# Performance work log

Measured on AMD Instinct MI355X. Metric: run time of the kernel, lower is better.

Reference implementation:

```python
import jax, jax.numpy as jnp
import numpy as np
import math

D_MODEL = 1024
N_HEADS = 16
HEAD_DIM = D_MODEL // N_HEADS


def setup_inputs() -> dict:
    key = jax.random.key(0)
    k1, k2, k3 = jax.random.split(key, 3)
    B, T = 2, 2048
    x = jax.random.normal(k1, (B, T, D_MODEL), dtype=jnp.float32)
    W_qkv = jax.random.normal(k2, (D_MODEL, 3 * D_MODEL), dtype=jnp.float32) * (1.0 / math.sqrt(D_MODEL))
    W_out = jax.random.normal(k3, (D_MODEL, D_MODEL), dtype=jnp.float32) * (1.0 / math.sqrt(D_MODEL))
    return {"x": x, "W_qkv": W_qkv, "W_out": W_out}


def reference(x, W_qkv, W_out):
    B, T, C = x.shape
    qkv = x @ W_qkv  # [B, T, 3C]
    q, k, v = jnp.split(qkv, 3, axis=-1)

    def heads(t):  # [B,T,C] -> [B,H,T,Dh]
        return t.reshape(B, T, N_HEADS, HEAD_DIM).transpose(0, 2, 1, 3)

    q, k, v = heads(q), heads(k), heads(v)
    scale = 1.0 / math.sqrt(HEAD_DIM)
    scores = jnp.einsum('bhtd,bhsd->bhts', q, k) * scale  # [B,H,T,T]
    causal = jnp.tril(jnp.ones((T, T), dtype=bool))
    scores = jnp.where(causal[None, None, :, :], scores, -jnp.inf)
    attn = jax.nn.softmax(scores, axis=-1)
    out = jnp.einsum('bhts,bhsd->bhtd', attn, v)  # [B,H,T,Dh]
    out = out.transpose(0, 2, 1, 3).reshape(B, T, C)
    return out @ W_out
```

## Files before the change

kernel.cpp:

```cpp
#include <hip/hip_runtime.h>
#include <hip/hip_bf16.h>

typedef __bf16 bf16;
typedef bf16 bf16x4 __attribute__((ext_vector_type(4)));
typedef bf16 bf16x8 __attribute__((ext_vector_type(8)));
typedef float f32x4 __attribute__((ext_vector_type(4)));
typedef float f32x16 __attribute__((ext_vector_type(16)));
typedef unsigned int u32x4 __attribute__((ext_vector_type(4)));

#define GLOAD16(g, l) __builtin_amdgcn_global_load_lds( \
    (const __attribute__((address_space(1))) void*)(g),  \
    (__attribute__((address_space(3))) void*)(l), 16, 0, 0)

#define EXP2F(x) __builtin_amdgcn_exp2f(x)
#define MFMA16(a, b, c) __builtin_amdgcn_mfma_f32_16x16x32_bf16(a, b, c, 0, 0, 0)
#define MFMA32(a, b, c) __builtin_amdgcn_mfma_f32_32x32x16_bf16(a, b, c, 0, 0, 0)

__global__ __launch_bounds__(256) void prep(const float* __restrict__ x,
                                            const float* __restrict__ Wqkv,
                                            const float* __restrict__ Wout,
                                            bf16* __restrict__ xb,
                                            bf16* __restrict__ wqkvT,
                                            bf16* __restrict__ woutT) {
  int id = blockIdx.x, tid = threadIdx.x;
  if (id < 2048) {
    int i = id * 256 + tid;
    const float4* p = (const float4*)x + (size_t)i * 2;
    float4 a = p[0], b = p[1];
    bf16x8 o;
    o[0] = (bf16)a.x; o[1] = (bf16)a.y; o[2] = (bf16)a.z; o[3] = (bf16)a.w;
    o[4] = (bf16)b.x; o[5] = (bf16)b.y; o[6] = (bf16)b.z; o[7] = (bf16)b.w;
    ((bf16x8*)xb)[i] = o;
  } else {
    __shared__ float tile[32][33];
    const float* src; bf16* dst; int N, j;
    if (id < 5120) { src = Wqkv; dst = wqkvT; N = 3072; j = id - 2048; }
    else           { src = Wout; dst = woutT; N = 1024; j = id - 5120; }
    int ntile = N / 32;
    int n0 = (j % ntile) * 32, k0 = (j / ntile) * 32;
    int tx = tid & 31, ty = tid >> 5;
#pragma unroll
    for (int i = 0; i < 4; i++)
      tile[ty + 8 * i][tx] = src[(size_t)(k0 + ty + 8 * i) * N + n0 + tx];
    __syncthreads();
#pragma unroll
    for (int i = 0; i < 4; i++)
      dst[(size_t)(n0 + ty + 8 * i) * 1024 + k0 + tx] = (bf16)tile[tx][ty + 8 * i];
  }
}

__device__ __forceinline__ void gemm_mainloop64(const bf16* __restrict__ A,
                                                const bf16* __restrict__ Bt,
                                                int K, int m0, int n0,
                                                f32x4 acc[4][4],
                                                bf16* As, bf16* Bs) {
  int tid = threadIdx.x;
  int lane = tid & 63;
  int wave = tid >> 6;
  int wr = wave >> 1, wc = wave & 1;
  int c16 = lane & 15, g = lane >> 4;
  f32x4 z = {0.f, 0.f, 0.f, 0.f};
#pragma unroll
  for (int m = 0; m < 4; m++)
#pragma unroll
    for (int n = 0; n < 4; n++) acc[m][n] = z;
  for (int k0 = 0; k0 < K; k0 += 64) {
#pragma unroll
    for (int i = 0; i < 4; i++) {
      int cc = tid + i * 256;
      int r = cc >> 3, ch = cc & 7;
      int sc = ch ^ (r & 7);
      GLOAD16(A + (size_t)(m0 + r) * K + k0 + sc * 8, As + cc * 8);
    }
#pragma unroll
    for (int i = 0; i < 4; i++) {
      int cc = tid + i * 256;
      int r = cc >> 3, ch = cc & 7;
      int sc = ch ^ (r & 7);
      GLOAD16(Bt + (size_t)(n0 + r) * K + k0 + sc * 8, Bs + cc * 8);
    }
    __syncthreads();
#pragma unroll
    for (int h = 0; h < 2; h++) {
      bf16x8 af[4], bfr[4];
#pragma unroll
      for (int m = 0; m < 4; m++) {
        int ar = wr * 64 + m * 16 + c16;
        af[m] = *(const bf16x8*)((const char*)As + ar * 128 + (((h * 4 + g) ^ (ar & 7)) << 4));
      }
#pragma unroll
      for (int n = 0; n < 4; n++) {
        int br = wc * 64 + n * 16 + c16;
        bfr[n] = *(const bf16x8*)((const char*)Bs + br * 128 + (((h * 4 + g) ^ (br & 7)) << 4));
      }
      __builtin_amdgcn_s_setprio(1);
#pragma unroll
      for (int m = 0; m < 4; m++)
#pragma unroll
        for (int n = 0; n < 4; n++)
          acc[m][n] = MFMA16(af[m], bfr[n], acc[m][n]);
      __builtin_amdgcn_s_setprio(0);
    }
    __syncthreads();
  }
}

__global__ __launch_bounds__(256) void gemm_qkv(const bf16* __restrict__ A,
                                                const bf16* __restrict__ Bt,
                                                bf16* __restrict__ q,
                                                bf16* __restrict__ kk,
                                                bf16* __restrict__ vt) {
  __shared__ bf16 As[128 * 64];
  __shared__ bf16 Bs[128 * 64];
  int id = blockIdx.x;
  int xc = id & 7, k = id >> 3;
  int bn = xc * 3 + (k % 3), bm = k / 3;
  int m0 = bm * 128, n0 = bn * 128;
  f32x4 acc[4][4];
  gemm_mainloop64(A, Bt, 1024, m0, n0, acc, As, Bs);
  int lane = threadIdx.x & 63;
  int wave = threadIdx.x >> 6;
  int wr = wave >> 1, wc = wave & 1;
  int c16 = lane & 15, g = lane >> 4;
  int which = n0 >> 10;
  const float QSCALE = 0.125f * 1.4426950408889634f;
  if (which == 2) {
#pragma unroll
    for (int m = 0; m < 4; m++)
#pragma unroll
      for (int n = 0; n < 4; n++) {
        int gm0 = m0 + wr * 64 + m * 16 + g * 4;
        int gn = n0 + wc * 64 + n * 16 + c16;
        int rem = gn & 1023, h = rem >> 6, d = rem & 63;
        int b = gm0 >> 11, t0 = gm0 & 2047;
        size_t bh = (size_t)(b * 16 + h);
        bf16x4 pv;
        pv[0] = (bf16)acc[m][n][0]; pv[1] = (bf16)acc[m][n][1];
        pv[2] = (bf16)acc[m][n][2]; pv[3] = (bf16)acc[m][n][3];
        *(bf16x4*)(vt + (bh * 64 + d) * 2048 + t0) = pv;
      }
  } else {
#pragma unroll
    for (int m = 0; m < 4; m++)
#pragma unroll
      for (int n = 0; n < 4; n++)
#pragma unroll
        for (int j = 0; j < 4; j++) {
          int gm = m0 + wr * 64 + m * 16 + g * 4 + j;
          int gn = n0 + wc * 64 + n * 16 + c16;
          int rem = gn & 1023, h = rem >> 6, d = rem & 63;
          int b = gm >> 11, t = gm & 2047;
          float v = acc[m][n][j];
          size_t bh = (size_t)(b * 16 + h);
          if (which == 0) q[(bh * 2048 + t) * 64 + d]  = (bf16)(v * QSCALE);
          else            kk[(bh * 2048 + t) * 64 + d] = (bf16)v;
        }
  }
}

__global__ __launch_bounds__(256) void gemm_out(const bf16* __restrict__ A,
                                                const bf16* __restrict__ Bt,
                                                float* __restrict__ C) {
  __shared__ bf16 As[64 * 64];
  __shared__ bf16 Bs[128 * 64];
  int tid = threadIdx.x;
  int lane = tid & 63;
  int wave = tid >> 6;
  int wr = wave >> 1, wc = wave & 1;
  int c16 = lane & 15, g = lane >> 4;
  int id = blockIdx.x;
  int bn = id & 7, bm = id >> 3;
  int m0 = bm * 64, n0 = bn * 128;
  const int K = 1024;
  f32x4 acc[2][4];
  {
    f32x4 z = {0.f, 0.f, 0.f, 0.f};
#pragma unroll
    for (int m = 0; m < 2; m++)
#pragma unroll
      for (int n = 0; n < 4; n++) acc[m][n] = z;
  }
  for (int k0 = 0; k0 < K; k0 += 64) {
#pragma unroll
    for (int i = 0; i < 2; i++) {
      int cc = tid + i * 256;
      int r = cc >> 3, ch = cc & 7;
      int sc = ch ^ (r & 7);
      GLOAD16(A + (size_t)(m0 + r) * K + k0 + sc * 8, As + cc * 8);
    }
#pragma unroll
    for (int i = 0; i < 4; i++) {
      int cc = tid + i * 256;
      int r = cc >> 3, ch = cc & 7;
      int sc = ch ^ (r & 7);
      GLOAD16(Bt + (size_t)(n0 + r) * K + k0 + sc * 8, Bs + cc * 8);
    }
    __syncthreads();
#pragma unroll
    for (int h = 0; h < 2; h++) {
      bf16x8 af[2], bfr[4];
#pragma unroll
      for (int m = 0; m < 2; m++) {
        int ar = wr * 32 + m * 16 + c16;
        af[m] = *(const bf16x8*)((const char*)As + ar * 128 + (((h * 4 + g) ^ (ar & 7)) << 4));
      }
#pragma unroll
      for (int n = 0; n < 4; n++) {
        int br = wc * 64 + n * 16 + c16;
        bfr[n] = *(const bf16x8*)((const char*)Bs + br * 128 + (((h * 4 + g) ^ (br & 7)) << 4));
      }
      __builtin_amdgcn_s_setprio(1);
#pragma unroll
      for (int m = 0; m < 2; m++)
#pragma unroll
        for (int n = 0; n < 4; n++)
          acc[m][n] = MFMA16(af[m], bfr[n], acc[m][n]);
      __builtin_amdgcn_s_setprio(0);
    }
    __syncthreads();
  }
#pragma unroll
  for (int m = 0; m < 2; m++)
#pragma unroll
    for (int n = 0; n < 4; n++)
#pragma unroll
      for (int j = 0; j < 4; j++) {
        int gm = m0 + wr * 32 + m * 16 + g * 4 + j;
        int gn = n0 + wc * 64 + n * 16 + c16;
        C[(size_t)gm * 1024 + gn] = acc[m][n][j];
      }
}

__global__ __launch_bounds__(512, 4) void attn(const bf16* __restrict__ q,
                                               const bf16* __restrict__ kk,
                                               const bf16* __restrict__ vt,
                                               bf16* __restrict__ out) {
  __shared__ __align__(16) char smem[65536];
  bf16* Ks = (bf16*)smem;
  bf16* Vs = (bf16*)(smem + 32768);
  int tid = threadIdx.x, lane = tid & 63, w = tid >> 6;
  int qw = w & 3, par = w >> 2;
  int ql = lane & 31, hi = lane >> 5;

  int id = blockIdx.x;
  int c = id & 7;
  int k = id >> 3;
  int s = k >> 5;
  int j5 = k & 31;
  int bxi = j5 & 15, b2 = j5 >> 4;
  int bx = s ? (15 - bxi) : bxi;
  int bh = 4 * c + 2 * b2 + s;
  int q0 = bx * 128;

  const bf16* qb = q  + (size_t)bh * 2048 * 64;
  const bf16* kb = kk + (size_t)bh * 2048 * 64;
  const bf16* vb = vt + (size_t)bh * 64 * 2048;
  int nt = 2 * bx + 2;
  int ns = nt >> 1;

  int qlo = q0 + qw * 32;
  int qg = qlo + ql;

  bf16x8 qf[4];
#pragma unroll
  for (int j = 0; j < 4; j++)
    qf[j] = *(const bf16x8*)(qb + (size_t)qg * 64 + j * 16 + hi * 8);

  {
    int cc = tid;
    int r = cc >> 3;
    int sw = ((cc & 7) ^ (r & 7)) * 8;
    GLOAD16(kb + (size_t)r * 64 + sw, Ks + cc * 8);
    GLOAD16(vb + (size_t)r * 2048 + sw, Vs + cc * 8);
    GLOAD16(kb + (size_t)(64 + r) * 64 + sw, Ks + 4096 + cc * 8);
    GLOAD16(vb + (size_t)r * 2048 + 64 + sw, Vs + 4096 + cc * 8);
  }
  __syncthreads();

  f32x16 o[2];
#pragma unroll
  for (int i = 0; i < 16; i++) { o[0][i] = 0.f; o[1][i] = 0.f; }
  float lsum = 0.f;

  for (int st = 0; st < ns; ++st) {
    if (st + 1 < ns) {
      int sn = st * 128 + 128;
      int nb = (2 * st + 2) & 3;
      int cc = tid;
      int r = cc >> 3;
      int sw = ((cc & 7) ^ (r & 7)) * 8;
      GLOAD16(kb + (size_t)(sn + r) * 64 + sw, Ks + nb * 4096 + cc * 8);
      GLOAD16(vb + (size_t)r * 2048 + sn + sw, Vs + nb * 4096 + cc * 8);
      GLOAD16(kb + (size_t)(sn + 64 + r) * 64 + sw, Ks + (nb + 1) * 4096 + cc * 8);
      GLOAD16(vb + (size_t)r * 2048 + sn + 64 + sw, Vs + (nb + 1) * 4096 + cc * 8);
    }
    int t = 2 * st + par;
    int s0 = t * 64;
    if (s0 <= qlo + 31) {
      const char* Kb = (const char*)(Ks + (t & 3) * 4096);
      const char* Vb = (const char*)(Vs + (t & 3) * 4096);
      f32x16 S[2];
#pragma unroll
      for (int i = 0; i < 16; i++) { S[0][i] = 0.f; S[1][i] = 0.f; }
      __builtin_amdgcn_s_setprio(1);
#pragma unroll
      for (int j = 0; j < 4; j++) {
        int row0 = ql, row1 = 32 + ql;
        bf16x8 kf0 = *(const bf16x8*)(Kb + row0 * 128 + (((2 * j + hi) ^ (row0 & 7)) << 4));
        bf16x8 kf1 = *(const bf16x8*)(Kb + row1 * 128 + (((2 * j + hi) ^ (row1 & 7)) << 4));
        S[0] = MFMA32(kf0, qf[j], S[0]);
        S[1] = MFMA32(kf1, qf[j], S[1]);
      }
      __builtin_amdgcn_s_setprio(0);
      if (s0 + 63 > qlo) {
#pragma unroll
        for (int sb = 0; sb < 2; sb++)
#pragma unroll
          for (int r = 0; r < 16; r++) {
            int sg = s0 + sb * 32 + (r & 3) + 8 * (r >> 2) + 4 * hi;
            if (sg > qg) S[sb][r] = -__builtin_inff();
          }
      }
#pragma unroll
      for (int sb = 0; sb < 2; sb++)
#pragma unroll
        for (int r = 0; r < 16; r++) {
          float pv2 = EXP2F(S[sb][r]);
          S[sb][r] = pv2;
          lsum += pv2;
        }
      __builtin_amdgcn_s_setprio(1);
#pragma unroll
      for (int j = 0; j < 4; j++) {
        int sb = j >> 1, rb = (j & 1) * 8;
        unsigned pa, pb, pc, pd;
        asm("v_cvt_pk_bf16_f32 %0, %1, %2" : "=v"(pa) : "v"(S[sb][rb + 0]), "v"(S[sb][rb + 1]));
        asm("v_cvt_pk_bf16_f32 %0, %1, %2" : "=v"(pb) : "v"(S[sb][rb + 2]), "v"(S[sb][rb + 3]));
        asm("v_cvt_pk_bf16_f32 %0, %1, %2" : "=v"(pc) : "v"(S[sb][rb + 4]), "v"(S[sb][rb + 5]));
        asm("v_cvt_pk_bf16_f32 %0, %1, %2" : "=v"(pd) : "v"(S[sb][rb + 6]), "v"(S[sb][rb + 7]));
        asm("v_permlane32_swap_b32 %0, %1" : "+v"(pa), "+v"(pc));
        asm("v_permlane32_swap_b32 %0, %1" : "+v"(pb), "+v"(pd));
        union { u32x4 u; bf16x8 h; } pu;
        pu.u[0] = pa; pu.u[1] = pb; pu.u[2] = pc; pu.u[3] = pd;
        int row0 = ql, row1 = 32 + ql;
        bf16x8 vf0 = *(const bf16x8*)(Vb + row0 * 128 + (((2 * j + hi) ^ (row0 & 7)) << 4));
        bf16x8 vf1 = *(const bf16x8*)(Vb + row1 * 128 + (((2 * j + hi) ^ (row1 & 7)) << 4));
        o[0] = MFMA32(vf0, pu.h, o[0]);
        o[1] = MFMA32(vf1, pu.h, o[1]);
      }
      __builtin_amdgcn_s_setprio(0);
    }
    if (st + 1 < ns) {
      asm volatile("s_waitcnt vmcnt(0)" ::: "memory");
      __builtin_amdgcn_s_barrier();
      __builtin_amdgcn_sched_barrier(0);
    }
  }
  lsum += __shfl_xor(lsum, 32);
  __syncthreads();
  float* xch = (float*)smem;
  if (par == 1) {
    float* dst = xch + (qw * 64 + lane) * 33;
#pragma unroll
    for (int db = 0; db < 2; db++)
#pragma unroll
      for (int i = 0; i < 16; i++) dst[db * 16 + i] = o[db][i];
    dst[32] = lsum;
  }
  __syncthreads();
  if (par == 0) {
    const float* src = xch + (qw * 64 + lane) * 33;
#pragma unroll
    for (int db = 0; db < 2; db++)
#pragma unroll
      for (int i = 0; i < 16; i++) o[db][i] += src[db * 16 + i];
    lsum += src[32];
    float inv = 1.f / lsum;
    int b = bh >> 4, h = bh & 15;
    size_t rowbase = ((size_t)(b * 2048 + qg)) * 1024 + h * 64;
#pragma unroll
    for (int db = 0; db < 2; db++)
#pragma unroll
      for (int qd = 0; qd < 4; qd++) {
        bf16x4 pv;
#pragma unroll
        for (int i = 0; i < 4; i++) pv[i] = (bf16)(o[db][4 * qd + i] * inv);
        *(bf16x4*)(out + rowbase + db * 32 + 8 * qd + 4 * hi) = pv;
      }
  }
}

extern "C" void kernel_launch(void* const* d_in, const int* in_sizes, int n_in,
                              void* d_out, int out_size, void* d_ws, size_t ws_size,
                              hipStream_t stream) {
  const float* x    = (const float*)d_in[0];
  const float* Wqkv = (const float*)d_in[1];
  const float* Wout = (const float*)d_in[2];
  float* outp = (float*)d_out;
  char* ws = (char*)d_ws;
  const size_t MB = 1024 * 1024;
  bf16* xb    = (bf16*)(ws);
  bf16* wqkvT = (bf16*)(ws + 8 * MB);
  bf16* woutT = (bf16*)(ws + 14 * MB);
  bf16* qb    = (bf16*)(ws + 16 * MB);
  bf16* kb    = (bf16*)(ws + 24 * MB);
  bf16* vtb   = (bf16*)(ws + 32 * MB);

  hipLaunchKernelGGL(prep, dim3(6144), dim3(256), 0, stream,
                     x, Wqkv, Wout, xb, wqkvT, woutT);
  hipLaunchKernelGGL(gemm_qkv, dim3(768), dim3(256), 0, stream,
                     xb, wqkvT, qb, kb, vtb);
  hipLaunchKernelGGL(attn, dim3(512), dim3(512), 0, stream,
                     qb, kb, vtb, xb);
  hipLaunchKernelGGL(gemm_out, dim3(512), dim3(256), 0, stream,
                     xb, woutT, outp);
}
```

Before: 89.77 us.

## Rewrite QKV GEMM with 256x256 tiles and double-buffered LDS pipeline

Replaces the 128x128 single-buffered QKV GEMM with a 256x256-tile kernel using 512 threads, a 128KB double-buffered LDS ring and interleaved global-to-LDS prefetch of the next K slice during MFMA work. Barriers are placed per quarter-step, with vmcnt waits only at slot boundaries. This cuts the grid from 768 to 192 blocks and remaps blocks to XCDs. It raises reuse per tile and overlaps loads with compute, but 192 blocks may underfill the 256 CUs, and the larger register and LDS footprint lowers occupancy.

```diff
diff --git a/kernel.cpp b/kernel.cpp
--- a/kernel.cpp
+++ b/kernel.cpp
@@ -49,108 +49,136 @@
   }
 }
 
-__device__ __forceinline__ void gemm_mainloop64(const bf16* __restrict__ A,
-                                                const bf16* __restrict__ Bt,
-                                                int K, int m0, int n0,
-                                                f32x4 acc[4][4],
-                                                bf16* As, bf16* Bs) {
-  int tid = threadIdx.x;
-  int lane = tid & 63;
-  int wave = tid >> 6;
-  int wr = wave >> 1, wc = wave & 1;
+__global__ __launch_bounds__(512, 2) void gemm_qkv(const bf16* __restrict__ A,
+                                                   const bf16* __restrict__ Bt,
+                                                   bf16* __restrict__ q,
+                                                   bf16* __restrict__ kk,
+                                                   bf16* __restrict__ vt) {
+  __shared__ __align__(16) char smem[131072];
+  char* Asb = smem;
+  char* Bsb = smem + 65536;
+  int tid = threadIdx.x, lane = tid & 63, w = tid >> 6;
+  int wr = w >> 2, wc = w & 3;
   int c16 = lane & 15, g = lane >> 4;
-  f32x4 z = {0.f, 0.f, 0.f, 0.f};
-#pragma unroll
-  for (int m = 0; m < 4; m++)
-#pragma unroll
-    for (int n = 0; n < 4; n++) acc[m][n] = z;
-  for (int k0 = 0; k0 < K; k0 += 64) {
-#pragma unroll
-    for (int i = 0; i < 4; i++) {
-      int cc = tid + i * 256;
-      int r = cc >> 3, ch = cc & 7;
-      int sc = ch ^ (r & 7);
-      GLOAD16(A + (size_t)(m0 + r) * K + k0 + sc * 8, As + cc * 8);
-    }
-#pragma unroll
-    for (int i = 0; i < 4; i++) {
-      int cc = tid + i * 256;
-      int r = cc >> 3, ch = cc & 7;
-      int sc = ch ^ (r & 7);
-      GLOAD16(Bt + (size_t)(n0 + r) * K + k0 + sc * 8, Bs + cc * 8);
-    }
-    __syncthreads();
-#pragma unroll
-    for (int h = 0; h < 2; h++) {
-      bf16x8 af[4], bfr[4];
-#pragma unroll
-      for (int m = 0; m < 4; m++) {
-        int ar = wr * 64 + m * 16 + c16;
-        af[m] = *(const bf16x8*)((const char*)As + ar * 128 + (((h * 4 + g) ^ (ar & 7)) << 4));
-      }
-#pragma unroll
-      for (int n = 0; n < 4; n++) {
-        int br = wc * 64 + n * 16 + c16;
-        bfr[n] = *(const bf16x8*)((const char*)Bs + br * 128 + (((h * 4 + g) ^ (br & 7)) << 4));
+  int id = blockIdx.x;
+  int xcd = id & 7, kb = id >> 3;
+  int bm = (xcd >> 1) * 4 + (kb & 3);
+  int bn = (xcd & 1) * 6 + (kb >> 2);
+  int m0 = bm * 256, n0 = bn * 256;
+
+  auto stageKT = [&](int kt, int slot) {
+    int kcol = kt * 64;
+#pragma unroll
+    for (int ht = 0; ht < 2; ht++) {
+#pragma unroll
+      for (int li = 0; li < 2; li++) {
+        int cc = li * 512 + tid;
+        int rr = cc >> 3, ch = cc & 7;
+        int sw8 = (ch ^ (rr & 7)) * 8;
+        GLOAD16(A + (size_t)(m0 + ht * 128 + rr) * 1024 + kcol + sw8,
+                Asb + (slot * 2 + ht) * 16384 + cc * 16);
+        GLOAD16(Bt + (size_t)(n0 + ht * 128 + rr) * 1024 + kcol + sw8,
+                Bsb + (slot * 2 + ht) * 16384 + cc * 16);
+      }
+    }
+  };
+
+  int swk0 = (g ^ (c16 & 7)) << 4;
+  int swk1 = ((4 + g) ^ (c16 & 7)) << 4;
+  const char* Afb[2];
+  const char* Bfb[2];
+#pragma unroll
+  for (int s = 0; s < 2; s++) {
+    Afb[s] = Asb + (s * 2 + wr) * 16384 + c16 * 128;
+    Bfb[s] = Bsb + (s * 2 + (wc >> 1)) * 16384 + ((wc & 1) * 64 + c16) * 128;
+  }
+
+  f32x4 acc[8][4];
+  {
+    f32x4 z = {0.f, 0.f, 0.f, 0.f};
+#pragma unroll
+    for (int mi = 0; mi < 8; mi++)
+#pragma unroll
+      for (int ni = 0; ni < 4; ni++) acc[mi][ni] = z;
+  }
+
+  stageKT(0, 0);
+  asm volatile("s_waitcnt vmcnt(0)" ::: "memory");
+  __builtin_amdgcn_s_barrier();
+  __builtin_amdgcn_sched_barrier(0);
+
+  bf16x8 bfr[4][2];
+  for (int i = 0; i < 8; ++i) {
+#pragma unroll
+    for (int p = 0; p < 8; ++p) {
+      const int qd = p & 3;
+      const int slot = p >> 2;
+      if (p == 0) stageKT(2 * i + 1, 1);
+      else if (p == 4 && i < 7) stageKT(2 * i + 2, 0);
+      if (qd == 0) {
+#pragma unroll
+        for (int ni = 0; ni < 4; ni++) {
+          bfr[ni][0] = *(const bf16x8*)(Bfb[slot] + ni * 2048 + swk0);
+          bfr[ni][1] = *(const bf16x8*)(Bfb[slot] + ni * 2048 + swk1);
+        }
+      }
+      bf16x8 af0[2], af1[2];
+#pragma unroll
+      for (int mm = 0; mm < 2; mm++) {
+        af0[mm] = *(const bf16x8*)(Afb[slot] + (2 * qd + mm) * 2048 + swk0);
+        af1[mm] = *(const bf16x8*)(Afb[slot] + (2 * qd + mm) * 2048 + swk1);
       }
       __builtin_amdgcn_s_setprio(1);
 #pragma unroll
-      for (int m = 0; m < 4; m++)
-#pragma unroll
-        for (int n = 0; n < 4; n++)
-          acc[m][n] = MFMA16(af[m], bfr[n], acc[m][n]);
+      for (int mm = 0; mm < 2; mm++)
+#pragma unroll
+        for (int ni = 0; ni < 4; ni++)
+          acc[2 * qd + mm][ni] = MFMA16(af0[mm], bfr[ni][0], acc[2 * qd + mm][ni]);
+#pragma unroll
+      for (int mm = 0; mm < 2; mm++)
+#pragma unroll
+        for (int ni = 0; ni < 4; ni++)
+          acc[2 * qd + mm][ni] = MFMA16(af1[mm], bfr[ni][1], acc[2 * qd + mm][ni]);
       __builtin_amdgcn_s_setprio(0);
-    }
-    __syncthreads();
-  }
-}
-
-__global__ __launch_bounds__(256) void gemm_qkv(const bf16* __restrict__ A,
-                                                const bf16* __restrict__ Bt,
-                                                bf16* __restrict__ q,
-                                                bf16* __restrict__ kk,
-                                                bf16* __restrict__ vt) {
-  __shared__ bf16 As[128 * 64];
-  __shared__ bf16 Bs[128 * 64];
-  int id = blockIdx.x;
-  int xc = id & 7, k = id >> 3;
-  int bn = xc * 3 + (k % 3), bm = k / 3;
-  int m0 = bm * 128, n0 = bn * 128;
-  f32x4 acc[4][4];
-  gemm_mainloop64(A, Bt, 1024, m0, n0, acc, As, Bs);
-  int lane = threadIdx.x & 63;
-  int wave = threadIdx.x >> 6;
-  int wr = wave >> 1, wc = wave & 1;
-  int c16 = lane & 15, g = lane >> 4;
+      if (p == 3 || (p == 7 && i < 7)) {
+        asm volatile("s_waitcnt vmcnt(0)" ::: "memory");
+      }
+      if (!(p == 7 && i == 7)) {
+        __builtin_amdgcn_s_barrier();
+        __builtin_amdgcn_sched_barrier(0);
+      }
+    }
+  }
+
   int which = n0 >> 10;
   const float QSCALE = 0.125f * 1.4426950408889634f;
   if (which == 2) {
 #pragma unroll
-    for (int m = 0; m < 4; m++)
-#pragma unroll
-      for (int n = 0; n < 4; n++) {
-        int gm0 = m0 + wr * 64 + m * 16 + g * 4;
-        int gn = n0 + wc * 64 + n * 16 + c16;
+    for (int mi = 0; mi < 8; mi++)
+#pragma unroll
+      for (int ni = 0; ni < 4; ni++) {
+        int gm0 = m0 + wr * 128 + mi * 16 + g * 4;
+        int gn = n0 + wc * 64 + ni * 16 + c16;
         int rem = gn & 1023, h = rem >> 6, d = rem & 63;
         int b = gm0 >> 11, t0 = gm0 & 2047;
         size_t bh = (size_t)(b * 16 + h);
         bf16x4 pv;
-        pv[0] = (bf16)acc[m][n][0]; pv[1] = (bf16)acc[m][n][1];
-        pv[2] = (bf16)acc[m][n][2]; pv[3] = (bf16)acc[m][n][3];
+        pv[0] = (bf16)acc[mi][ni][0]; pv[1] = (bf16)acc[mi][ni][1];
+        pv[2] = (bf16)acc[mi][ni][2]; pv[3] = (bf16)acc[mi][ni][3];
         *(bf16x4*)(vt + (bh * 64 + d) * 2048 + t0) = pv;
       }
   } else {
 #pragma unroll
-    for (int m = 0; m < 4; m++)
-#pragma unroll
-      for (int n = 0; n < 4; n++)
+    for (int mi = 0; mi < 8; mi++)
+#pragma unroll
+      for (int ni = 0; ni < 4; ni++)
 #pragma unroll
         for (int j = 0; j < 4; j++) {
-          int gm = m0 + wr * 64 + m * 16 + g * 4 + j;
-          int gn = n0 + wc * 64 + n * 16 + c16;
+          int gm = m0 + wr * 128 + mi * 16 + g * 4 + j;
+          int gn = n0 + wc * 64 + ni * 16 + c16;
           int rem = gn & 1023, h = rem >> 6, d = rem & 63;
           int b = gm >> 11, t = gm & 2047;
-          float v = acc[m][n][j];
+          float v = acc[mi][ni][j];
           size_t bh = (size_t)(b * 16 + h);
           if (which == 0) q[(bh * 2048 + t) * 64 + d]  = (bf16)(v * QSCALE);
           else            kk[(bh * 2048 + t) * 64 + d] = (bf16)v;
@@ -408,7 +436,7 @@
 
   hipLaunchKernelGGL(prep, dim3(6144), dim3(256), 0, stream,
                      x, Wqkv, Wout, xb, wqkvT, woutT);
-  hipLaunchKernelGGL(gemm_qkv, dim3(768), dim3(256), 0, stream,
+  hipLaunchKernelGGL(gemm_qkv, dim3(192), dim3(512), 0, stream,
                      xb, wqkvT, qb, kb, vtb);
   hipLaunchKernelGGL(attn, dim3(512), dim3(512), 0, stream,
                      qb, kb, vtb, xb);
```

After: 93.24 us. 3.9% more time.
